# Performance work log

Hardware: AMD Instinct MI355X
Metric: run time of the kernel (lower is better)

## Reference

```python
import jax, jax.numpy as jnp
import numpy as np

SELU_SCALE = 1.0507009873554805
SELU_ALPHA = 1.6732632423543772

def _learned_activation(x, w):
    # softmax-blended mixture of 8 activations plus a zero 'linear' branch
    p = jax.nn.softmax(w)
    sig = jax.nn.sigmoid(x)
    elu = jax.nn.elu(x)
    tanh = jnp.tanh(x)
    relu = jax.nn.relu(x)
    silu = jax.nn.silu(x)
    gelu = jax.nn.gelu(x, approximate=False)
    selu = SELU_SCALE * jnp.where(x > 0, x, SELU_ALPHA * jnp.expm1(x))
    mish = x * jnp.tanh(jax.nn.softplus(x))
    return (p[0] * sig + p[1] * elu + p[2] * tanh + p[3] * relu
            + p[4] * silu + p[5] * gelu + p[6] * selu + p[7] * mish)  # p[8]*0 (linear=0)


def setup_inputs() -> dict:
    key = jax.random.key(0)
    ks = jax.random.split(key, 10)
    B, D, H, E, M = 1024, 1024, 2048, 8, 2048
    init_units = 1024
    s = lambda fan_in: 1.0 / np.sqrt(fan_in)
    x = jax.random.normal(ks[0], (B, D), jnp.float32)
    gate_w = jax.random.normal(ks[1], (D, E), jnp.float32) * s(D)
    expert_w = jax.random.normal(ks[2], (E, D, H), jnp.float32) * s(D)
    expert_b = jnp.zeros((E, H), jnp.float32)
    conn_w1 = jax.random.normal(ks[3], (E, H, 32), jnp.float32) * s(H)
    conn_b1 = jnp.zeros((E, 32), jnp.float32)
    conn_w2 = jax.random.normal(ks[4], (E, 32, H), jnp.float32) * s(32)
    conn_b2 = jnp.zeros((E, H), jnp.float32)
    neuron_avg = jax.random.uniform(ks[5], (E, H), jnp.float32)
    # initial mask: first initial_units neurons active per expert
    neuron_mask = jnp.tile(
        jnp.concatenate([jnp.ones((init_units,), jnp.float32),
                         jnp.zeros((H - init_units,), jnp.float32)])[None, :], (E, 1))
    mem_read_w = jax.random.normal(ks[6], (H, M), jnp.float32) * s(H)
    mem_read_b = jnp.zeros((M,), jnp.float32)
    memory = jax.random.normal(ks[7], (M, H), jnp.float32) * s(M)
    act_w = jnp.ones((9,), jnp.float32)
    return {"x": x, "gate_w": gate_w, "expert_w": expert_w, "expert_b": expert_b,
            "conn_w1": conn_w1, "conn_b1": conn_b1, "conn_w2": conn_w2, "conn_b2": conn_b2,
            "neuron_avg": neuron_avg, "neuron_mask": neuron_mask,
            "mem_read_w": mem_read_w, "mem_read_b": mem_read_b,
            "memory": memory, "act_w": act_w}


def reference(x, gate_w, expert_w, expert_b, conn_w1, conn_b1, conn_w2, conn_b2,
              neuron_avg, neuron_mask, mem_read_w, mem_read_b, memory, act_w):
    # --- MoE gate over experts ---
    gate = jax.nn.softmax(x @ gate_w, axis=-1)  # [B, E]
    # --- DynamicConnectivity soft gating, per expert (from neuron_activation_avg) ---
    h1 = jax.nn.relu(jnp.einsum('eh,ehk->ek', neuron_avg, conn_w1) + conn_b1)  # [E, 32]
    conn = jax.nn.sigmoid(jnp.einsum('ek,ekh->eh', h1, conn_w2) + conn_b2)     # [E, H]
    # --- plastic dense experts: z -> gated -> masked -> relu ---
    z = jnp.einsum('bd,edh->ebh', x, expert_w) + expert_b[:, None, :]  # [E, B, H]
    a = jax.nn.relu(z * (conn * neuron_mask)[:, None, :])              # [E, B, H]
    moe_out = jnp.einsum('be,ebh->bh', gate, a)                        # [B, H]
    # --- episodic memory read (attention over memory slots) ---
    attn = jax.nn.softmax(moe_out @ mem_read_w + mem_read_b, axis=-1)  # [B, M]
    read_vec = attn @ memory                                           # [B, H]
    # --- blended learned activation on residual sum ---
    return _learned_activation(moe_out + read_vec, act_w)
```

## Files before the change

### kernel.cpp

```cpp
#include <hip/hip_runtime.h>
#include <hip/hip_bf16.h>
#include <math.h>

typedef __bf16 bf16_t;
typedef __bf16 bf16x8 __attribute__((ext_vector_type(8)));
typedef __bf16 bf16x4 __attribute__((ext_vector_type(4)));
typedef float f32x4 __attribute__((ext_vector_type(4)));

#define B_DIM 1024
#define D_DIM 1024
#define H_DIM 2048
#define E_DIM 8
#define M_DIM 2048

typedef const __attribute__((address_space(1))) unsigned int as1_uint;
typedef __attribute__((address_space(3))) unsigned int as3_uint;

__device__ __forceinline__ void gl_lds16(const void* g, void* l) {
  __builtin_amdgcn_global_load_lds((as1_uint*)g, (as3_uint*)l, 16, 0, 0);
}

#define WAITV(n) asm volatile("s_waitcnt vmcnt(" #n ")" ::: "memory")

__global__ __launch_bounds__(256, 6) void prep_kernel(
    const float* __restrict__ ew, const float* __restrict__ mrw, const float* __restrict__ mem,
    bf16_t* __restrict__ wbT, bf16_t* __restrict__ mrT, bf16_t* __restrict__ memT,
    const float* __restrict__ x, const float* __restrict__ gw,
    float* __restrict__ gate_t, bf16_t* __restrict__ x_bf) {
  __shared__ char smem[16384];
  const int bid = blockIdx.x;
  const int t = threadIdx.x;

  if (bid < 3072) {
    bf16_t* tile = (bf16_t*)smem;
    const float* in; bf16_t* out; int R, C, rt, ct;
    if (bid < 2048) {
      int slab = bid >> 8, rem = bid & 255;
      in = ew + (size_t)slab * D_DIM * H_DIM; out = wbT + (size_t)slab * D_DIM * H_DIM;
      R = D_DIM; C = H_DIM; rt = rem >> 5; ct = rem & 31;
    } else if (bid < 2560) {
      int rem = bid - 2048;
      in = mrw; out = mrT; R = H_DIM; C = M_DIM; rt = rem >> 5; ct = rem & 31;
    } else {
      int rem = bid - 2560;
      in = mem; out = memT; R = M_DIM; C = H_DIM; rt = rem >> 5; ct = rem & 31;
    }
    const int r0 = rt * 128, c0 = ct * 64;
    int cq = (t & 15) * 4, rr = t >> 4;
#pragma unroll
    for (int i = 0; i < 8; ++i) {
      int r = rr + 16 * i;
      float4 v = *(const float4*)&in[(size_t)(r0 + r) * C + c0 + cq];
      bf16x4 b;
      b[0] = (bf16_t)v.x; b[1] = (bf16_t)v.y; b[2] = (bf16_t)v.z; b[3] = (bf16_t)v.w;
      *(bf16x4*)&tile[r * 64 + (cq ^ (((r >> 3) & 7) << 2))] = b;
    }
    __syncthreads();
    int r8 = (t & 15) * 8, cc = t >> 4;
    const int sw = (t & 7) << 2;
#pragma unroll
    for (int i = 0; i < 4; ++i) {
      int c = cc + 16 * i;
      bf16x8 o;
#pragma unroll
      for (int j = 0; j < 8; ++j) o[j] = tile[(r8 + j) * 64 + (c ^ sw)];
      *(bf16x8*)&out[(size_t)(c0 + c) * R + r0 + r8] = o;
    }
  } else {
    float (*red)[8] = (float(*)[8])smem;
    int b = bid - 3072;
    float4 v = ((const float4*)(x + (size_t)b * D_DIM))[t];
    bf16x4 xb;
    xb[0] = (bf16_t)v.x; xb[1] = (bf16_t)v.y; xb[2] = (bf16_t)v.z; xb[3] = (bf16_t)v.w;
    *(bf16x4*)&x_bf[(size_t)b * D_DIM + t * 4] = xb;
    float acc[8];
#pragma unroll
    for (int e = 0; e < 8; ++e)
      acc[e] = v.x * gw[(4 * t) * 8 + e] + v.y * gw[(4 * t + 1) * 8 + e] +
               v.z * gw[(4 * t + 2) * 8 + e] + v.w * gw[(4 * t + 3) * 8 + e];
#pragma unroll
    for (int e = 0; e < 8; ++e) red[t][e] = acc[e];
    __syncthreads();
    for (int s = 128; s > 0; s >>= 1) {
      if (t < s) {
#pragma unroll
        for (int e = 0; e < 8; ++e) red[t][e] += red[t + s][e];
      }
      __syncthreads();
    }
    if (t == 0) {
      float m = red[0][0];
#pragma unroll
      for (int e = 1; e < 8; ++e) m = fmaxf(m, red[0][e]);
      float p[8], sum = 0.f;
#pragma unroll
      for (int e = 0; e < 8; ++e) { p[e] = expf(red[0][e] - m); sum += p[e]; }
      float inv = 1.f / sum;
#pragma unroll
      for (int e = 0; e < 8; ++e) gate_t[e * B_DIM + b] = p[e] * inv;
    }
  }
}

__global__ __launch_bounds__(256) void conn_kernel(
    const float* __restrict__ avg, const float* __restrict__ w1, const float* __restrict__ b1,
    const float* __restrict__ w2, const float* __restrict__ b2,
    const float* __restrict__ mask, float* __restrict__ conn) {
  __shared__ float red[256 * 32];
  __shared__ float h1[32];
  int e = blockIdx.x >> 3, c = blockIdx.x & 7, t = threadIdx.x;
  float acc[32];
#pragma unroll
  for (int k = 0; k < 32; ++k) acc[k] = 0.f;
#pragma unroll
  for (int i = 0; i < 8; ++i) {
    int h = i * 256 + t;
    float av = avg[e * H_DIM + h];
    const float* w1p = &w1[((size_t)e * H_DIM + h) * 32];
#pragma unroll
    for (int k = 0; k < 32; ++k) acc[k] += av * w1p[k];
  }
#pragma unroll
  for (int k = 0; k < 32; ++k) red[t * 32 + k] = acc[k];
  __syncthreads();
  for (int s = 128; s > 0; s >>= 1) {
    if (t < s) {
#pragma unroll
      for (int k = 0; k < 32; ++k) red[t * 32 + k] += red[(t + s) * 32 + k];
    }
    __syncthreads();
  }
  if (t < 32) h1[t] = fmaxf(red[t] + b1[e * 32 + t], 0.f);
  __syncthreads();
  int h = c * 256 + t;
  float s = b2[e * H_DIM + h];
#pragma unroll
  for (int k = 0; k < 32; ++k) s += h1[k] * w2[((size_t)e * 32 + k) * H_DIM + h];
  conn[e * H_DIM + h] = (1.f / (1.f + expf(-s))) * mask[e * H_DIM + h];
}

__global__ __launch_bounds__(512, 2) void expert_gemm(
    const bf16_t* __restrict__ A, const bf16_t* __restrict__ Bt,
    float* __restrict__ moe, bf16_t* __restrict__ moebf,
    const float* __restrict__ gate_t, const float* __restrict__ conn,
    const float* __restrict__ ebias) {
  __shared__ bf16_t As[2][128 * 64];
  __shared__ bf16_t Bs[8][64 * 64];

  const int wid = (blockIdx.x & 7) * 32 + (blockIdx.x >> 3);
  const int b0 = (wid & 7) * 128;
  const int n0 = (wid >> 3) * 64;

  const int t = threadIdx.x;
  const int lane = t & 63, wave = t >> 6;
  const int wmh = wave >> 2, wnq = wave & 3;
  const int lr = lane & 15, lk = (lane >> 4) * 8;
  const int csw = (lr & 7) << 3;
  const int srow = lane >> 3;
  const int scol = ((lane & 7) ^ srow) << 3;
  const size_t EB = (size_t)H_DIM * D_DIM;

  const bf16_t* Asrc = A + (size_t)(b0 + wave * 16 + srow) * D_DIM + scol;
  const bf16_t* Bsrc = Bt + (size_t)(n0 + wave * 8 + srow) * D_DIM + scol;

  auto stageA = [&](int buf, int kt) {
    gl_lds16(Asrc + (size_t)kt * 64, &As[buf][(wave * 16) * 64]);
    gl_lds16(Asrc + 8 * D_DIM + (size_t)kt * 64, &As[buf][(wave * 16 + 8) * 64]);
  };
  auto stageB = [&](int slot, int e, int kt) {
    gl_lds16(Bsrc + (size_t)e * EB + (size_t)kt * 64, &Bs[slot][(wave * 8) * 64]);
  };
  auto readB = [&](int slot, bf16x8& r0, bf16x8& r1) {
    const bf16_t* Bb = &Bs[slot][0];
    r0 = *(const bf16x8*)&Bb[(wnq * 16 + lr) * 64 + (lk ^ csw)];
    r1 = *(const bf16x8*)&Bb[(wnq * 16 + lr) * 64 + ((32 + lk) ^ csw)];
  };

  f32x4 acc[8][4];
#pragma unroll
  for (int e = 0; e < 8; ++e)
#pragma unroll
    for (int mf = 0; mf < 4; ++mf) acc[e][mf] = (f32x4){0.f, 0.f, 0.f, 0.f};

  stageA(0, 0);
  stageB(0, 0, 0);
  stageB(1, 1, 0);
  stageB(2, 2, 0);
  stageB(3, 3, 0);

  for (int kt = 0; kt < 16; ++kt) {
    const int ab = kt & 1;
    const bool last = (kt == 15);
    bf16x8 af[2][4];
#pragma unroll
    for (int eh = 0; eh < 4; ++eh) {
      const int e0 = eh * 2, e1 = e0 + 1;
      if (eh < 2) {
        stageB(e0 + 4, e0 + 4, kt);
        stageB(e1 + 4, e1 + 4, kt);
      } else if (!last) {
        stageB(e0 - 4, e0 - 4, kt + 1);
        stageB(e1 - 4, e1 - 4, kt + 1);
        if (eh == 2) stageA(ab ^ 1, kt + 1);
      }
      if (eh < 2)        { WAITV(4); }
      else if (!last)    { WAITV(6); }
      else if (eh == 2)  { WAITV(2); }
      else               { WAITV(0); }
      __builtin_amdgcn_s_barrier();
      __builtin_amdgcn_sched_barrier(0);
      if (eh == 0) {
#pragma unroll
        for (int kk = 0; kk < 2; ++kk)
#pragma unroll
          for (int mf = 0; mf < 4; ++mf)
            af[kk][mf] = *(const bf16x8*)&As[ab][(wmh * 64 + mf * 16 + lr) * 64 +
                                                ((kk * 32 + lk) ^ csw)];
      }
      bf16x8 p0, p1, q0, q1;
      readB(e0, p0, p1);
      readB(e1, q0, q1);
      __builtin_amdgcn_s_setprio(1);
#pragma unroll
      for (int mf = 0; mf < 4; ++mf) {
        acc[e0][mf] = __builtin_amdgcn_mfma_f32_16x16x32_bf16(af[0][mf], p0, acc[e0][mf], 0, 0, 0);
        acc[e0][mf] = __builtin_amdgcn_mfma_f32_16x16x32_bf16(af[1][mf], p1, acc[e0][mf], 0, 0, 0);
      }
#pragma unroll
      for (int mf = 0; mf < 4; ++mf) {
        acc[e1][mf] = __builtin_amdgcn_mfma_f32_16x16x32_bf16(af[0][mf], q0, acc[e1][mf], 0, 0, 0);
        acc[e1][mf] = __builtin_amdgcn_mfma_f32_16x16x32_bf16(af[1][mf], q1, acc[e1][mf], 0, 0, 0);
      }
      __builtin_amdgcn_s_setprio(0);
    }
  }

  const int r4 = (lane >> 4) * 4;
  const int gcol = n0 + wnq * 16 + lr;
  const int growb = b0 + wmh * 64;
  f32x4 sum[4];
#pragma unroll
  for (int mf = 0; mf < 4; ++mf) sum[mf] = (f32x4){0.f, 0.f, 0.f, 0.f};
#pragma unroll
  for (int e = 0; e < 8; ++e) {
    const float cm = conn[e * H_DIM + gcol];
    const float bb = ebias[e * H_DIM + gcol];
#pragma unroll
    for (int mf = 0; mf < 4; ++mf) {
      const float4 g4 = *(const float4*)&gate_t[e * B_DIM + growb + mf * 16 + r4];
      sum[mf][0] += fmaxf((acc[e][mf][0] + bb) * cm, 0.f) * g4.x;
      sum[mf][1] += fmaxf((acc[e][mf][1] + bb) * cm, 0.f) * g4.y;
      sum[mf][2] += fmaxf((acc[e][mf][2] + bb) * cm, 0.f) * g4.z;
      sum[mf][3] += fmaxf((acc[e][mf][3] + bb) * cm, 0.f) * g4.w;
    }
  }
#pragma unroll
  for (int mf = 0; mf < 4; ++mf)
#pragma unroll
    for (int j = 0; j < 4; ++j) {
      const int grow = growb + mf * 16 + r4 + j;
      moe[(size_t)grow * H_DIM + gcol] = sum[mf][j];
      moebf[(size_t)grow * H_DIM + gcol] = (bf16_t)sum[mf][j];
    }
}

__global__ __launch_bounds__(512, 2) void gemm_sk4(
    const bf16_t* __restrict__ A, const bf16_t* __restrict__ Bt, float* __restrict__ C) {
  __shared__ bf16_t As[2][128 * 64];
  __shared__ bf16_t Bs[2][128 * 64];

  const int wid = (blockIdx.x & 7) * 64 + (blockIdx.x >> 3);
  const int ez = wid >> 7;
  const int rem = wid & 127;
  const int b0 = (rem & 7) * 128;
  const int n0 = (rem >> 3) * 128;
  const int kbase = ez << 9;

  const int t = threadIdx.x;
  const int lane = t & 63, wave = t >> 6;
  const int wm = wave >> 2, wn = wave & 3;
  const int lr = lane & 15, lk = (lane >> 4) * 8;
  const int csw = (lr & 7) << 3;
  const int srow = lane >> 3;
  const int scol = ((lane & 7) ^ srow) << 3;

  const bf16_t* Arow = A + (size_t)(b0 + srow) * 2048 + kbase + scol;
  const bf16_t* Brow = Bt + (size_t)(n0 + srow) * 2048 + kbase + scol;

  const f32x4 zv = {0.f, 0.f, 0.f, 0.f};
  f32x4 acc[4][2];
#pragma unroll
  for (int mf = 0; mf < 4; ++mf)
#pragma unroll
    for (int nf = 0; nf < 2; ++nf) acc[mf][nf] = zv;

  auto STAGE = [&](int bsel, int kt) {
    const int ko = kt << 6;
#pragma unroll
    for (int i = 0; i < 2; ++i) {
      int rb = i * 64 + wave * 8;
      gl_lds16(Arow + (size_t)rb * 2048 + ko, &As[bsel][rb * 64]);
      gl_lds16(Brow + (size_t)rb * 2048 + ko, &Bs[bsel][rb * 64]);
    }
  };

  auto COMPUTE = [&](int bsel) {
    bf16x8 bfr[2][2];
#pragma unroll
    for (int kk = 0; kk < 2; ++kk)
#pragma unroll
      for (int nf = 0; nf < 2; ++nf)
        bfr[kk][nf] = *(const bf16x8*)&Bs[bsel][(wn * 32 + nf * 16 + lr) * 64 + ((kk * 32 + lk) ^ csw)];
    __builtin_amdgcn_s_setprio(1);
#pragma unroll
    for (int mf = 0; mf < 4; ++mf) {
      bf16x8 a0 = *(const bf16x8*)&As[bsel][(wm * 64 + mf * 16 + lr) * 64 + (lk ^ csw)];
      bf16x8 a1 = *(const bf16x8*)&As[bsel][(wm * 64 + mf * 16 + lr) * 64 + ((32 + lk) ^ csw)];
#pragma unroll
      for (int nf = 0; nf < 2; ++nf)
        acc[mf][nf] = __builtin_amdgcn_mfma_f32_16x16x32_bf16(a0, bfr[0][nf], acc[mf][nf], 0, 0, 0);
#pragma unroll
      for (int nf = 0; nf < 2; ++nf)
        acc[mf][nf] = __builtin_amdgcn_mfma_f32_16x16x32_bf16(a1, bfr[1][nf], acc[mf][nf], 0, 0, 0);
    }
    __builtin_amdgcn_s_setprio(0);
  };

  STAGE(0, 0);
  __syncthreads();
  for (int kt = 0; kt < 7; ++kt) {
    STAGE((kt + 1) & 1, kt + 1);
    COMPUTE(kt & 1);
    __syncthreads();
  }
  COMPUTE(1);

  const int r4 = (lane >> 4) * 4;
#pragma unroll
  for (int mf = 0; mf < 4; ++mf) {
#pragma unroll
    for (int nf = 0; nf < 2; ++nf) {
      int gcol = n0 + wn * 32 + nf * 16 + lr;
#pragma unroll
      for (int j = 0; j < 4; ++j) {
        int grow = b0 + wm * 64 + mf * 16 + r4 + j;
        C[((size_t)ez * B_DIM + grow) * 2048 + gcol] = acc[mf][nf][j];
      }
    }
  }
}

__global__ __launch_bounds__(256) void softmax_kernel(
    const float* __restrict__ lg, const float* __restrict__ bias, bf16_t* __restrict__ attn) {
  const size_t P = (size_t)B_DIM * M_DIM;
  int b = blockIdx.x, t = threadIdx.x;
  int lane = t & 63, wave = t >> 6;
  __shared__ float rmax[4], rsum[4];
  float v[8];
  float m = -1e30f;
#pragma unroll
  for (int i = 0; i < 8; ++i) {
    size_t idx = (size_t)b * M_DIM + i * 256 + t;
    v[i] = lg[idx] + lg[P + idx] + lg[2 * P + idx] + lg[3 * P + idx] + bias[i * 256 + t];
    m = fmaxf(m, v[i]);
  }
#pragma unroll
  for (int off = 32; off >= 1; off >>= 1) m = fmaxf(m, __shfl_xor(m, off));
  if (lane == 0) rmax[wave] = m;
  __syncthreads();
  m = fmaxf(fmaxf(rmax[0], rmax[1]), fmaxf(rmax[2], rmax[3]));
  float s = 0.f;
#pragma unroll
  for (int i = 0; i < 8; ++i) {
    v[i] = __expf(v[i] - m);
    s += v[i];
  }
#pragma unroll
  for (int off = 32; off >= 1; off >>= 1) s += __shfl_xor(s, off);
  if (lane == 0) rsum[wave] = s;
  __syncthreads();
  s = rsum[0] + rsum[1] + rsum[2] + rsum[3];
  float inv = 1.f / s;
#pragma unroll
  for (int i = 0; i < 8; ++i) attn[(size_t)b * M_DIM + i * 256 + t] = (bf16_t)(v[i] * inv);
}

__global__ __launch_bounds__(256) void act_kernel(
    const float* __restrict__ rdv, const float* __restrict__ aw, float* __restrict__ out) {
  const size_t P = (size_t)B_DIM * H_DIM;
  int i = blockIdx.x * 256 + threadIdx.x;
  float w[9], m = -1e30f;
#pragma unroll
  for (int j = 0; j < 9; ++j) { w[j] = aw[j]; m = fmaxf(m, w[j]); }
  float p[9], s = 0.f;
#pragma unroll
  for (int j = 0; j < 9; ++j) { p[j] = expf(w[j] - m); s += p[j]; }
  float inv = 1.f / s;
#pragma unroll
  for (int j = 0; j < 9; ++j) p[j] *= inv;
  float4 mv = ((const float4*)out)[i];
  float4 r0 = ((const float4*)rdv)[i];
  float4 r1 = ((const float4*)(rdv + P))[i];
  float4 r2 = ((const float4*)(rdv + 2 * P))[i];
  float4 r3 = ((const float4*)(rdv + 3 * P))[i];
  float xs[4] = {mv.x + r0.x + r1.x + r2.x + r3.x, mv.y + r0.y + r1.y + r2.y + r3.y,
                 mv.z + r0.z + r1.z + r2.z + r3.z, mv.w + r0.w + r1.w + r2.w + r3.w};
  float os[4];
#pragma unroll
  for (int q = 0; q < 4; ++q) {
    float xv = xs[q];
    float enx = expf(-xv);
    float ex = expf(xv);
    float sig = 1.f / (1.f + enx);
    float em1 = expm1f(xv);
    float th = tanhf(xv);
    float rl = fmaxf(xv, 0.f);
    float si = xv * sig;
    float ge = 0.5f * xv * (1.f + erff(xv * 0.70710678118654752f));
    float se = 1.0507009873554805f * (xv > 0.f ? xv : 1.6732632423543772f * em1);
    float el = xv > 0.f ? xv : em1;
    float sp = log1pf(ex);
    float mi = xv * tanhf(sp);
    os[q] = p[0] * sig + p[1] * el + p[2] * th + p[3] * rl + p[4] * si + p[5] * ge + p[6] * se + p[7] * mi;
  }
  ((float4*)out)[i] = make_float4(os[0], os[1], os[2], os[3]);
}

extern "C" void kernel_launch(void* const* d_in, const int* in_sizes, int n_in,
                              void* d_out, int out_size, void* d_ws, size_t ws_size,
                              hipStream_t stream) {
  const float* x        = (const float*)d_in[0];
  const float* gate_w   = (const float*)d_in[1];
  const float* expert_w = (const float*)d_in[2];
  const float* expert_b = (const float*)d_in[3];
  const float* conn_w1  = (const float*)d_in[4];
  const float* conn_b1  = (const float*)d_in[5];
  const float* conn_w2  = (const float*)d_in[6];
  const float* conn_b2  = (const float*)d_in[7];
  const float* navg     = (const float*)d_in[8];
  const float* nmask    = (const float*)d_in[9];
  const float* mem_rw   = (const float*)d_in[10];
  const float* mem_rb   = (const float*)d_in[11];
  const float* memory   = (const float*)d_in[12];
  const float* act_w    = (const float*)d_in[13];
  float* out = (float*)d_out;

  char* ws = (char*)d_ws;
  bf16_t* wbT    = (bf16_t*)(ws + 0);
  bf16_t* mrT    = (bf16_t*)(ws + 33554432);
  bf16_t* memT   = (bf16_t*)(ws + 41943040);
  float*  gate_t = (float*)(ws + 50331648);
  float*  connb  = (float*)(ws + 50364416);
  bf16_t* x_bf   = (bf16_t*)(ws + 50429952);
  bf16_t* moe_bf = (bf16_t*)(ws + 52527104);
  float*  logits = (float*)(ws + 0);
  bf16_t* attn   = (bf16_t*)(ws + 33554432);
  float*  readv  = (float*)(ws + 0);
  float*  moe    = out;

  prep_kernel<<<dim3(4096), 256, 0, stream>>>(expert_w, mem_rw, memory, wbT, mrT, memT,
                                              x, gate_w, gate_t, x_bf);
  conn_kernel<<<dim3(64), 256, 0, stream>>>(navg, conn_w1, conn_b1, conn_w2, conn_b2, nmask, connb);
  expert_gemm<<<dim3(256), 512, 0, stream>>>(x_bf, wbT, moe, moe_bf, gate_t, connb, expert_b);
  gemm_sk4<<<dim3(512), 512, 0, stream>>>(moe_bf, mrT, logits);
  softmax_kernel<<<dim3(B_DIM), 256, 0, stream>>>(logits, mem_rb, attn);
  gemm_sk4<<<dim3(512), 512, 0, stream>>>(attn, memT, readv);
  act_kernel<<<dim3((B_DIM * H_DIM) / (256 * 4)), 256, 0, stream>>>(readv, act_w, out);
}
```

Baseline: 137.0 us.

## Merge conn into prep kernel, enlarge transpose tiles, switch to split-K 2 GEMMs

Folds the connectivity kernel into the prep kernel, saving one launch and letting its blocks run alongside the transposes. Each transpose block now converts a 512x64 tile through 64KB of LDS instead of 128x64, cutting the block count but lowering occupancy. The memory-read GEMMs go from split-K 4 with 128x128 tiles to split-K 2 with 128x64 tiles. That halves the fp32 partial buffers that softmax and act_kernel must read, but each block now runs a longer K loop.

Result: faster. 129.7 us (-5.3%).

```diff
diff --git a/kernel.cpp b/kernel.cpp
--- a/kernel.cpp
+++ b/kernel.cpp
@@ -22,53 +22,57 @@
 
 #define WAITV(n) asm volatile("s_waitcnt vmcnt(" #n ")" ::: "memory")
 
-__global__ __launch_bounds__(256, 6) void prep_kernel(
+__global__ __launch_bounds__(256) void prep_kernel(
     const float* __restrict__ ew, const float* __restrict__ mrw, const float* __restrict__ mem,
     bf16_t* __restrict__ wbT, bf16_t* __restrict__ mrT, bf16_t* __restrict__ memT,
     const float* __restrict__ x, const float* __restrict__ gw,
-    float* __restrict__ gate_t, bf16_t* __restrict__ x_bf) {
-  __shared__ char smem[16384];
+    float* __restrict__ gate_t, bf16_t* __restrict__ x_bf,
+    const float* __restrict__ avg, const float* __restrict__ w1, const float* __restrict__ b1,
+    const float* __restrict__ w2, const float* __restrict__ b2,
+    const float* __restrict__ mask, float* __restrict__ conn) {
+  __shared__ char smem[65536];
   const int bid = blockIdx.x;
   const int t = threadIdx.x;
 
-  if (bid < 3072) {
+  if (bid < 768) {
     bf16_t* tile = (bf16_t*)smem;
     const float* in; bf16_t* out; int R, C, rt, ct;
-    if (bid < 2048) {
-      int slab = bid >> 8, rem = bid & 255;
+    if (bid < 512) {
+      int slab = bid >> 6, rem = bid & 63;
       in = ew + (size_t)slab * D_DIM * H_DIM; out = wbT + (size_t)slab * D_DIM * H_DIM;
       R = D_DIM; C = H_DIM; rt = rem >> 5; ct = rem & 31;
-    } else if (bid < 2560) {
-      int rem = bid - 2048;
+    } else if (bid < 640) {
+      int rem = bid - 512;
       in = mrw; out = mrT; R = H_DIM; C = M_DIM; rt = rem >> 5; ct = rem & 31;
     } else {
-      int rem = bid - 2560;
+      int rem = bid - 640;
       in = mem; out = memT; R = M_DIM; C = H_DIM; rt = rem >> 5; ct = rem & 31;
     }
-    const int r0 = rt * 128, c0 = ct * 64;
-    int cq = (t & 15) * 4, rr = t >> 4;
-#pragma unroll
-    for (int i = 0; i < 8; ++i) {
+    const int r0 = rt * 512, c0 = ct * 64;
+    const int cq = (t & 15) * 4, rr = t >> 4;
+#pragma unroll
+    for (int i = 0; i < 32; ++i) {
       int r = rr + 16 * i;
       float4 v = *(const float4*)&in[(size_t)(r0 + r) * C + c0 + cq];
       bf16x4 b;
       b[0] = (bf16_t)v.x; b[1] = (bf16_t)v.y; b[2] = (bf16_t)v.z; b[3] = (bf16_t)v.w;
-      *(bf16x4*)&tile[r * 64 + (cq ^ (((r >> 3) & 7) << 2))] = b;
+      *(bf16x4*)&tile[r * 64 + (cq ^ (((r >> 3) & 7) << 3))] = b;
     }
     __syncthreads();
-    int r8 = (t & 15) * 8, cc = t >> 4;
-    const int sw = (t & 7) << 2;
-#pragma unroll
-    for (int i = 0; i < 4; ++i) {
-      int c = cc + 16 * i;
+#pragma unroll
+    for (int i = 0; i < 16; ++i) {
+      int chunk = i * 256 + t;
+      int c = chunk >> 6;
+      int rc = (chunk & 63) * 8;
+      const int sw = ((chunk & 63) & 7) << 3;
       bf16x8 o;
 #pragma unroll
-      for (int j = 0; j < 8; ++j) o[j] = tile[(r8 + j) * 64 + (c ^ sw)];
-      *(bf16x8*)&out[(size_t)(c0 + c) * R + r0 + r8] = o;
-    }
-  } else {
+      for (int j = 0; j < 8; ++j) o[j] = tile[(rc + j) * 64 + (c ^ sw)];
+      *(bf16x8*)&out[(size_t)(c0 + c) * R + r0 + rc] = o;
+    }
+  } else if (bid < 1792) {
     float (*red)[8] = (float(*)[8])smem;
-    int b = bid - 3072;
+    int b = bid - 768;
     float4 v = ((const float4*)(x + (size_t)b * D_DIM))[t];
     bf16x4 xb;
     xb[0] = (bf16_t)v.x; xb[1] = (bf16_t)v.y; xb[2] = (bf16_t)v.z; xb[3] = (bf16_t)v.w;
@@ -99,44 +103,39 @@
 #pragma unroll
       for (int e = 0; e < 8; ++e) gate_t[e * B_DIM + b] = p[e] * inv;
     }
-  }
-}
-
-__global__ __launch_bounds__(256) void conn_kernel(
-    const float* __restrict__ avg, const float* __restrict__ w1, const float* __restrict__ b1,
-    const float* __restrict__ w2, const float* __restrict__ b2,
-    const float* __restrict__ mask, float* __restrict__ conn) {
-  __shared__ float red[256 * 32];
-  __shared__ float h1[32];
-  int e = blockIdx.x >> 3, c = blockIdx.x & 7, t = threadIdx.x;
-  float acc[32];
-#pragma unroll
-  for (int k = 0; k < 32; ++k) acc[k] = 0.f;
-#pragma unroll
-  for (int i = 0; i < 8; ++i) {
-    int h = i * 256 + t;
-    float av = avg[e * H_DIM + h];
-    const float* w1p = &w1[((size_t)e * H_DIM + h) * 32];
-#pragma unroll
-    for (int k = 0; k < 32; ++k) acc[k] += av * w1p[k];
-  }
-#pragma unroll
-  for (int k = 0; k < 32; ++k) red[t * 32 + k] = acc[k];
-  __syncthreads();
-  for (int s = 128; s > 0; s >>= 1) {
-    if (t < s) {
-#pragma unroll
-      for (int k = 0; k < 32; ++k) red[t * 32 + k] += red[(t + s) * 32 + k];
-    }
+  } else {
+    float* red = (float*)smem;
+    __shared__ float h1[32];
+    int e = (bid - 1792) >> 3, c = (bid - 1792) & 7;
+    float acc[32];
+#pragma unroll
+    for (int k = 0; k < 32; ++k) acc[k] = 0.f;
+#pragma unroll
+    for (int i = 0; i < 8; ++i) {
+      int h = i * 256 + t;
+      float av = avg[e * H_DIM + h];
+      const float* w1p = &w1[((size_t)e * H_DIM + h) * 32];
+#pragma unroll
+      for (int k = 0; k < 32; ++k) acc[k] += av * w1p[k];
+    }
+#pragma unroll
+    for (int k = 0; k < 32; ++k) red[t * 32 + k] = acc[k];
     __syncthreads();
-  }
-  if (t < 32) h1[t] = fmaxf(red[t] + b1[e * 32 + t], 0.f);
-  __syncthreads();
-  int h = c * 256 + t;
-  float s = b2[e * H_DIM + h];
-#pragma unroll
-  for (int k = 0; k < 32; ++k) s += h1[k] * w2[((size_t)e * 32 + k) * H_DIM + h];
-  conn[e * H_DIM + h] = (1.f / (1.f + expf(-s))) * mask[e * H_DIM + h];
+    for (int s = 128; s > 0; s >>= 1) {
+      if (t < s) {
+#pragma unroll
+        for (int k = 0; k < 32; ++k) red[t * 32 + k] += red[(t + s) * 32 + k];
+      }
+      __syncthreads();
+    }
+    if (t < 32) h1[t] = fmaxf(red[t] + b1[e * 32 + t], 0.f);
+    __syncthreads();
+    int h = c * 256 + t;
+    float s = b2[e * H_DIM + h];
+#pragma unroll
+    for (int k = 0; k < 32; ++k) s += h1[k] * w2[((size_t)e * 32 + k) * H_DIM + h];
+    conn[e * H_DIM + h] = (1.f / (1.f + expf(-s))) * mask[e * H_DIM + h];
+  }
 }
 
 __global__ __launch_bounds__(512, 2) void expert_gemm(
@@ -264,71 +263,68 @@
     }
 }
 
-__global__ __launch_bounds__(512, 2) void gemm_sk4(
+__global__ __launch_bounds__(512, 2) void gemm_sk2(
     const bf16_t* __restrict__ A, const bf16_t* __restrict__ Bt, float* __restrict__ C) {
   __shared__ bf16_t As[2][128 * 64];
-  __shared__ bf16_t Bs[2][128 * 64];
+  __shared__ bf16_t Bs[2][64 * 64];
 
   const int wid = (blockIdx.x & 7) * 64 + (blockIdx.x >> 3);
-  const int ez = wid >> 7;
-  const int rem = wid & 127;
+  const int ez = wid >> 8;
+  const int rem = wid & 255;
   const int b0 = (rem & 7) * 128;
-  const int n0 = (rem >> 3) * 128;
-  const int kbase = ez << 9;
+  const int n0 = (rem >> 3) * 64;
+  const int kbase = ez << 10;
 
   const int t = threadIdx.x;
   const int lane = t & 63, wave = t >> 6;
-  const int wm = wave >> 2, wn = wave & 3;
+  const int wm = wave >> 1, wn = wave & 1;
   const int lr = lane & 15, lk = (lane >> 4) * 8;
   const int csw = (lr & 7) << 3;
   const int srow = lane >> 3;
   const int scol = ((lane & 7) ^ srow) << 3;
 
-  const bf16_t* Arow = A + (size_t)(b0 + srow) * 2048 + kbase + scol;
-  const bf16_t* Brow = Bt + (size_t)(n0 + srow) * 2048 + kbase + scol;
+  const bf16_t* Arow = A + (size_t)(b0 + wave * 16 + srow) * 2048 + kbase + scol;
+  const bf16_t* Brow = Bt + (size_t)(n0 + wave * 8 + srow) * 2048 + kbase + scol;
 
   const f32x4 zv = {0.f, 0.f, 0.f, 0.f};
-  f32x4 acc[4][2];
-#pragma unroll
-  for (int mf = 0; mf < 4; ++mf)
+  f32x4 acc[2][2];
+#pragma unroll
+  for (int mf = 0; mf < 2; ++mf)
 #pragma unroll
     for (int nf = 0; nf < 2; ++nf) acc[mf][nf] = zv;
 
   auto STAGE = [&](int bsel, int kt) {
     const int ko = kt << 6;
-#pragma unroll
-    for (int i = 0; i < 2; ++i) {
-      int rb = i * 64 + wave * 8;
-      gl_lds16(Arow + (size_t)rb * 2048 + ko, &As[bsel][rb * 64]);
-      gl_lds16(Brow + (size_t)rb * 2048 + ko, &Bs[bsel][rb * 64]);
-    }
+    gl_lds16(Arow + ko, &As[bsel][(wave * 16) * 64]);
+    gl_lds16(Arow + (size_t)8 * 2048 + ko, &As[bsel][(wave * 16 + 8) * 64]);
+    gl_lds16(Brow + ko, &Bs[bsel][(wave * 8) * 64]);
   };
 
   auto COMPUTE = [&](int bsel) {
-    bf16x8 bfr[2][2];
-#pragma unroll
-    for (int kk = 0; kk < 2; ++kk)
+    bf16x8 bfr[2][2], afr[2][2];
+#pragma unroll
+    for (int kk = 0; kk < 2; ++kk) {
 #pragma unroll
       for (int nf = 0; nf < 2; ++nf)
         bfr[kk][nf] = *(const bf16x8*)&Bs[bsel][(wn * 32 + nf * 16 + lr) * 64 + ((kk * 32 + lk) ^ csw)];
+#pragma unroll
+      for (int mf = 0; mf < 2; ++mf)
+        afr[kk][mf] = *(const bf16x8*)&As[bsel][(wm * 32 + mf * 16 + lr) * 64 + ((kk * 32 + lk) ^ csw)];
+    }
     __builtin_amdgcn_s_setprio(1);
 #pragma unroll
-    for (int mf = 0; mf < 4; ++mf) {
-      bf16x8 a0 = *(const bf16x8*)&As[bsel][(wm * 64 + mf * 16 + lr) * 64 + (lk ^ csw)];
-      bf16x8 a1 = *(const bf16x8*)&As[bsel][(wm * 64 + mf * 16 + lr) * 64 + ((32 + lk) ^ csw)];
-#pragma unroll
-      for (int nf = 0; nf < 2; ++nf)
-        acc[mf][nf] = __builtin_amdgcn_mfma_f32_16x16x32_bf16(a0, bfr[0][nf], acc[mf][nf], 0, 0, 0);
-#pragma unroll
-      for (int nf = 0; nf < 2; ++nf)
-        acc[mf][nf] = __builtin_amdgcn_mfma_f32_16x16x32_bf16(a1, bfr[1][nf], acc[mf][nf], 0, 0, 0);
-    }
+    for (int mf = 0; mf < 2; ++mf)
+#pragma unroll
+      for (int nf = 0; nf < 2; ++nf) {
+        acc[mf][nf] = __builtin_amdgcn_mfma_f32_16x16x32_bf16(afr[0][mf], bfr[0][nf], acc[mf][nf], 0, 0, 0);
+        acc[mf][nf] = __builtin_amdgcn_mfma_f32_16x16x32_bf16(afr[1][mf], bfr[1][nf], acc[mf][nf], 0, 0, 0);
+      }
     __builtin_amdgcn_s_setprio(0);
   };
 
   STAGE(0, 0);
   __syncthreads();
-  for (int kt = 0; kt < 7; ++kt) {
+  for (int kt = 0; kt < 15; ++kt) {
     STAGE((kt + 1) & 1, kt + 1);
     COMPUTE(kt & 1);
     __syncthreads();
@@ -337,13 +333,13 @@
 
   const int r4 = (lane >> 4) * 4;
 #pragma unroll
-  for (int mf = 0; mf < 4; ++mf) {
+  for (int mf = 0; mf < 2; ++mf) {
 #pragma unroll
     for (int nf = 0; nf < 2; ++nf) {
       int gcol = n0 + wn * 32 + nf * 16 + lr;
 #pragma unroll
       for (int j = 0; j < 4; ++j) {
-        int grow = b0 + wm * 64 + mf * 16 + r4 + j;
+        int grow = b0 + wm * 32 + mf * 16 + r4 + j;
         C[((size_t)ez * B_DIM + grow) * 2048 + gcol] = acc[mf][nf][j];
       }
     }
@@ -361,7 +357,7 @@
 #pragma unroll
   for (int i = 0; i < 8; ++i) {
     size_t idx = (size_t)b * M_DIM + i * 256 + t;
-    v[i] = lg[idx] + lg[P + idx] + lg[2 * P + idx] + lg[3 * P + idx] + bias[i * 256 + t];
+    v[i] = lg[idx] + lg[P + idx] + bias[i * 256 + t];
     m = fmaxf(m, v[i]);
   }
 #pragma unroll
@@ -401,10 +397,8 @@
   float4 mv = ((const float4*)out)[i];
   float4 r0 = ((const float4*)rdv)[i];
   float4 r1 = ((const float4*)(rdv + P))[i];
-  float4 r2 = ((const float4*)(rdv + 2 * P))[i];
-  float4 r3 = ((const float4*)(rdv + 3 * P))[i];
-  float xs[4] = {mv.x + r0.x + r1.x + r2.x + r3.x, mv.y + r0.y + r1.y + r2.y + r3.y,
-                 mv.z + r0.z + r1.z + r2.z + r3.z, mv.w + r0.w + r1.w + r2.w + r3.w};
+  float xs[4] = {mv.x + r0.x + r1.x, mv.y + r0.y + r1.y,
+                 mv.z + r0.z + r1.z, mv.w + r0.w + r1.w};
   float os[4];
 #pragma unroll
   for (int q = 0; q < 4; ++q) {
@@ -454,16 +448,17 @@
   bf16_t* x_bf   = (bf16_t*)(ws + 50429952);
   bf16_t* moe_bf = (bf16_t*)(ws + 52527104);
   float*  logits = (float*)(ws + 0);
-  bf16_t* attn   = (bf16_t*)(ws + 33554432);
+  bf16_t* attn   = (bf16_t*)(ws + 16777216);
   float*  readv  = (float*)(ws + 0);
   float*  moe    = out;
 
-  prep_kernel<<<dim3(4096), 256, 0, stream>>>(expert_w, mem_rw, memory, wbT, mrT, memT,
-                                              x, gate_w, gate_t, x_bf);
-  conn_kernel<<<dim3(64), 256, 0, stream>>>(navg, conn_w1, conn_b1, conn_w2, conn_b2, nmask, connb);
+  prep_kernel<<<dim3(1856), 256, 0, stream>>>(expert_w, mem_rw, memory, wbT, mrT, memT,
+                                              x, gate_w, gate_t, x_bf,
+                                              navg, conn_w1, conn_b1, conn_w2, conn_b2,
+                                              nmask, connb);
   expert_gemm<<<dim3(256), 512, 0, stream>>>(x_bf, wbT, moe, moe_bf, gate_t, connb, expert_b);
-  gemm_sk4<<<dim3(512), 512, 0, stream>>>(moe_bf, mrT, logits);
+  gemm_sk2<<<dim3(512), 512, 0, stream>>>(moe_bf, mrT, logits);
   softmax_kernel<<<dim3(B_DIM), 256, 0, stream>>>(logits, mem_rb, attn);
-  gemm_sk4<<<dim3(512), 512, 0, stream>>>(attn, memT, readv);
+  gemm_sk2<<<dim3(512), 512, 0, stream>>>(attn, memT, readv);
   act_kernel<<<dim3((B_DIM * H_DIM) / (256 * 4)), 256, 0, stream>>>(readv, act_w, out);
 }
```
